# Kernel optimization log

Hardware: AMD Instinct MI355X
Metric: run time of the kernel (lower is better)

## Reference

```python
import jax, jax.numpy as jnp
import numpy as np
from jax import lax

B, S, D, NH, K = 4, 2048, 1024, 16, 3
EPS = 1e-6


def custom_layernorm(x, gamma, beta):
    # torch-style: std with ddof=1, eps added to std (not var)
    mean = jnp.mean(x, axis=-1, keepdims=True)
    var = jnp.sum((x - mean) ** 2, axis=-1, keepdims=True) / (x.shape[-1] - 1)
    std = jnp.sqrt(var)
    return gamma * ((x - mean) / (std + EPS)) + beta


def setup_inputs() -> dict:
    key = jax.random.key(0)
    ks = jax.random.split(key, 10)
    s = 1.0 / np.sqrt(D)
    return {
        "x": jax.random.normal(ks[0], (B, S, D), jnp.float32),
        "Wq": jax.random.normal(ks[1], (D, D), jnp.float32) * s,
        "bq": jax.random.normal(ks[2], (D,), jnp.float32) * 0.02,
        "Wk": jax.random.normal(ks[3], (D, D), jnp.float32) * s,
        "Wv": jax.random.normal(ks[4], (D, D), jnp.float32) * s,
        "bv": jax.random.normal(ks[5], (D,), jnp.float32) * 0.02,
        "conv_w": jax.random.normal(ks[6], (D, D // NH, K), jnp.float32) * (1.0 / np.sqrt((D // NH) * K)),
        "conv_b": jax.random.normal(ks[7], (D,), jnp.float32) * 0.02,
        "gamma": jnp.ones((D,), jnp.float32),
        "beta": jnp.zeros((D,), jnp.float32),
        "Wo": jax.random.normal(ks[8], (D, D), jnp.float32) * s,
        "bo": jax.random.normal(ks[9], (D,), jnp.float32) * 0.02,
    }


def reference(x, Wq, bq, Wk, Wv, bv, conv_w, conv_b, gamma, beta, Wo, bo):
    d = x.shape[-1]
    groups = d // conv_w.shape[1]
    pad = conv_w.shape[2] // 2

    q = x @ Wq + bq
    k = x @ Wk  # key has no bias
    v = x @ Wv + bv

    # grouped conv1d over sequence dim (NCW layout)
    xc = jnp.transpose(x, (0, 2, 1))  # [B, D, S]
    conv_out = lax.conv_general_dilated(
        xc, conv_w, window_strides=(1,), padding=[(pad, pad)],
        feature_group_count=groups,
        dimension_numbers=("NCH", "OIH", "NCH"),
    ) + conv_b[None, :, None]
    conv_out = jnp.transpose(conv_out, (0, 2, 1))  # [B, S, D]
    conv_out = custom_layernorm(conv_out, gamma, beta)  # dropout = identity (eval)

    scale = 1.0 / jnp.sqrt(jnp.asarray(d, x.dtype))
    scores = jnp.einsum("bqd,bkd->bqk", q, k) * scale  # [B, S, S]
    attn = jax.nn.softmax(scores, axis=-1)
    attention_out = jnp.einsum("bqk,bkd->bqd", attn, v)

    combined = custom_layernorm(conv_out + attention_out, gamma, beta)
    return combined @ Wo + bo + x
```

## Files before the change

kernel.cpp:

```cpp
#include <hip/hip_runtime.h>
#include <cstdint>


#define DEV __device__ __forceinline__

typedef unsigned short u16;
typedef __attribute__((ext_vector_type(8))) short bf16x8;
typedef __attribute__((ext_vector_type(4))) float f32x4;

static const int Sn = 2048, Dn = 1024;

DEV float bf2f(u16 u) { union { unsigned int i; float f; } w; w.i = ((unsigned int)u) << 16; return w.f; }
DEV u16 f2bf(float f) {
  union { float f; unsigned int i; } w; w.f = f;
  unsigned int x = w.i;
  return (u16)((x + 0x7FFFu + ((x >> 16) & 1u)) >> 16);
}

DEV void gload_lds16(const u16* gsrc, u16* lds_dst) {
  __builtin_amdgcn_global_load_lds(
      (const __attribute__((address_space(1))) void*)gsrc,
      (__attribute__((address_space(3))) void*)lds_dst,
      16, 0, 0);
}

DEV float block_allreduce_sum(float v, float* red, int tid) {
  #pragma unroll
  for (int o = 32; o > 0; o >>= 1) v += __shfl_down(v, o, 64);
  __syncthreads();
  if ((tid & 63) == 0) red[tid >> 6] = v;
  __syncthreads();
  return red[0] + red[1] + red[2] + red[3];
}

DEV float block_allreduce_max(float v, float* red, int tid) {
  #pragma unroll
  for (int o = 32; o > 0; o >>= 1) v = fmaxf(v, __shfl_down(v, o, 64));
  __syncthreads();
  if ((tid & 63) == 0) red[tid >> 6] = v;
  __syncthreads();
  return fmaxf(fmaxf(red[0], red[1]), fmaxf(red[2], red[3]));
}

__global__ __launch_bounds__(256)
void prep_all(const float* __restrict__ Wq, const float* __restrict__ Wk,
              const float* __restrict__ Wv, const float* __restrict__ Wo,
              u16* __restrict__ wT,
              const float* __restrict__ bq, const float* __restrict__ bv,
              float* __restrict__ qkvb,
              const float* __restrict__ cw, u16* __restrict__ wconv,
              const float* __restrict__ x, u16* __restrict__ xb) {
  __shared__ u16 sm[64][68];
  int blk = blockIdx.x;
  int tid = threadIdx.x;
  if (blk < 1024) {
    int w = blk >> 8, t = blk & 255;
    const float* src = (w == 0) ? Wq : (w == 1) ? Wk : (w == 2) ? Wv : Wo;
    u16* dst = wT + (size_t)w * 1048576u;
    int i0 = (t >> 4) << 6, j0 = (t & 15) << 6;
    int tx = tid & 15, r0 = tid >> 4;
    #pragma unroll
    for (int rr = r0; rr < 64; rr += 16) {
      float4 v = *(const float4*)&src[(long)(i0 + rr) * 1024 + j0 + tx * 4];
      sm[rr][tx*4+0] = f2bf(v.x); sm[rr][tx*4+1] = f2bf(v.y);
      sm[rr][tx*4+2] = f2bf(v.z); sm[rr][tx*4+3] = f2bf(v.w);
    }
    __syncthreads();
    #pragma unroll
    for (int cc = r0; cc < 64; cc += 16) {
      ushort4 o;
      o.x = sm[tx*4+0][cc]; o.y = sm[tx*4+1][cc];
      o.z = sm[tx*4+2][cc]; o.w = sm[tx*4+3][cc];
      *(ushort4*)&dst[(long)(j0 + cc) * 1024 + i0 + tx * 4] = o;
    }
  } else if (blk < 1040) {
    int oc0 = (blk - 1024) * 64;
    for (int idx = tid; idx < 64 * 192; idx += 256) {
      int oc = oc0 + idx / 192; int k = idx % 192;
      int t = k >> 6, i = k & 63;
      wconv[(long)oc * 192 + k] = f2bf(cw[(long)oc * 192 + i * 3 + t]);
    }
  } else if (blk == 1040) {
    for (int j = tid; j < 3072; j += 256) {
      float v = 0.0f;
      if (j < 1024) v = bq[j];
      else if (j >= 2048) v = bv[j - 2048];
      qkvb[j] = v;
    }
  } else {
    int i = (blk - 1041) * 1024 + tid * 4;
    float4 v = *(const float4*)&x[i];
    ushort4 o;
    o.x = f2bf(v.x); o.y = f2bf(v.y); o.z = f2bf(v.z); o.w = f2bf(v.w);
    *(ushort4*)&xb[i] = o;
  }
}

template<typename CT>
__global__ __launch_bounds__(256, 2)
void gemm_nt(const u16* __restrict__ A, const u16* __restrict__ A2, long Abs, int lda,
             const u16* __restrict__ B, long Bbs, int ldb,
             CT* __restrict__ C, CT* __restrict__ C2, long Cbs, int ldc,
             int zsplit, int K, float scale,
             const float* __restrict__ bias, int bias_bs,
             const float* __restrict__ res, long Rbs, int ldr) {
  __shared__ u16 sA[2][128 * 32];
  __shared__ u16 sB[2][128 * 32];
  int tid = threadIdx.x;
  int lane = tid & 63, wv = tid >> 6;
  int quad = lane >> 4, lm = lane & 15;
  int wr = wv >> 1, wc = wv & 1;
  long m0 = (long)blockIdx.x * 128, n0 = (long)blockIdx.y * 128;
  int z = blockIdx.z;
  if (z >= zsplit) { A = A2 + (long)(z - zsplit) * Abs; C = C2 + (long)(z - zsplit) * Cbs; }
  else             { A = A  + (long)z * Abs;            C = C  + (long)z * Cbs; }
  B += (long)z * Bbs;
  if (res) res += (long)z * Rbs;

  f32x4 acc[4][4] = {};

  int srow = wv * 16 + (lane >> 2);
  int sch = (lane & 3) * 8;
  const u16* Ap = A + (m0 + srow) * (long)lda + sch;
  const u16* Bp = B + (n0 + srow) * (long)ldb + sch;
  const int lofs = wv * 16 * 32;

  for (int k0 = 0; k0 < K; k0 += 64) {
    #pragma unroll
    for (int h = 0; h < 2; h++) {
      int kh = k0 + h * 32;
      gload_lds16(Ap + kh, &sA[h][lofs]);
      gload_lds16(Ap + 64 * (long)lda + kh, &sA[h][lofs + 64 * 32]);
      gload_lds16(Bp + kh, &sB[h][lofs]);
      gload_lds16(Bp + 64 * (long)ldb + kh, &sB[h][lofs + 64 * 32]);
    }
    __syncthreads();
    #pragma unroll
    for (int h = 0; h < 2; h++) {
      bf16x8 af[4], bfr[4];
      #pragma unroll
      for (int mi = 0; mi < 4; mi++)
        af[mi] = *(const bf16x8*)&sA[h][(wr * 64 + mi * 16 + lm) * 32 + quad * 8];
      #pragma unroll
      for (int ni = 0; ni < 4; ni++)
        bfr[ni] = *(const bf16x8*)&sB[h][(wc * 64 + ni * 16 + lm) * 32 + quad * 8];
      #pragma unroll
      for (int mi = 0; mi < 4; mi++)
        #pragma unroll
        for (int ni = 0; ni < 4; ni++)
          acc[mi][ni] = __builtin_amdgcn_mfma_f32_16x16x32_bf16(af[mi], bfr[ni], acc[mi][ni], 0, 0, 0);
    }
    __syncthreads();
  }

  #pragma unroll
  for (int mi = 0; mi < 4; mi++) {
    #pragma unroll
    for (int ni = 0; ni < 4; ni++) {
      int col = (int)n0 + wc * 64 + ni * 16 + lm;
      float bv = bias ? bias[(long)z * bias_bs + col] : 0.0f;
      #pragma unroll
      for (int r = 0; r < 4; r++) {
        long rowg = m0 + wr * 64 + mi * 16 + quad * 4 + r;
        float v = acc[mi][ni][r] * scale + bv;
        if (res) v += res[rowg * (long)ldr + col];
        if constexpr (sizeof(CT) == 2) C[rowg * (long)ldc + col] = f2bf(v);
        else                           C[rowg * (long)ldc + col] = v;
      }
    }
  }
}

__global__ __launch_bounds__(256)
void mid_all(const u16* __restrict__ xb, const u16* __restrict__ wt,
             const float* __restrict__ cb, u16* __restrict__ convo,
             const u16* __restrict__ Vb, u16* __restrict__ vt) {
  __shared__ u16 smem[9360];
  int blk = blockIdx.x;
  int tid = threadIdx.x;
  if (blk < 1024) {
    u16 (*sx)[72] = (u16(*)[72])smem;
    int s0 = (blk & 15) * 128;
    int g = (blk >> 4) & 15;
    int b = blk >> 8;
    int lane = tid & 63, wv = tid >> 6;
    int quad = lane >> 4, lm = lane & 15;
    for (int idx = tid; idx < 130 * 16; idx += 256) {
      int r = idx >> 4, c4 = (idx & 15) * 4;
      int s = s0 - 1 + r;
      ushort4 v;
      if (s >= 0 && s < Sn) v = *(const ushort4*)&xb[((long)b * Sn + s) * Dn + g * 64 + c4];
      else { v.x = 0; v.y = 0; v.z = 0; v.w = 0; }
      *(ushort4*)&sx[r][c4] = v;
    }
    __syncthreads();
    f32x4 acc[2][4] = {};
    const u16* wg = wt + (long)g * 64 * 192;
    #pragma unroll
    for (int ks = 0; ks < 6; ks++) {
      int t = ks >> 1;
      int i0 = (ks & 1) * 32 + quad * 8;
      bf16x8 a0 = *(const bf16x8*)&sx[wv * 32 + lm + t][i0];
      bf16x8 a1 = *(const bf16x8*)&sx[wv * 32 + 16 + lm + t][i0];
      #pragma unroll
      for (int nf = 0; nf < 4; nf++) {
        bf16x8 bf = *(const bf16x8*)&wg[(nf * 16 + lm) * 192 + ks * 32 + quad * 8];
        acc[0][nf] = __builtin_amdgcn_mfma_f32_16x16x32_bf16(a0, bf, acc[0][nf], 0, 0, 0);
        acc[1][nf] = __builtin_amdgcn_mfma_f32_16x16x32_bf16(a1, bf, acc[1][nf], 0, 0, 0);
      }
    }
    #pragma unroll
    for (int mi = 0; mi < 2; mi++) {
      #pragma unroll
      for (int nf = 0; nf < 4; nf++) {
        int col = g * 64 + nf * 16 + lm;
        float bias = cb[col];
        #pragma unroll
        for (int r = 0; r < 4; r++) {
          int row = wv * 32 + mi * 16 + quad * 4 + r;
          convo[((long)b * Sn + s0 + row) * Dn + col] = f2bf(acc[mi][nf][r] + bias);
        }
      }
    }
  } else {
    u16 (*sm)[68] = (u16(*)[68])smem;
    int t = blk - 1024;
    int b = t >> 9, r = t & 511;
    int j0 = (r & 15) << 6, i0 = ((r >> 4) & 31) << 6;
    const u16* s = Vb + (long)b * Sn * Dn;
    u16* d = vt + (long)b * Dn * Sn;
    int tx = tid & 15, r0 = tid >> 4;
    #pragma unroll
    for (int rr = r0; rr < 64; rr += 16) {
      ushort4 v = *(const ushort4*)&s[(long)(i0 + rr) * 1024 + j0 + tx * 4];
      sm[rr][tx*4+0] = v.x; sm[rr][tx*4+1] = v.y; sm[rr][tx*4+2] = v.z; sm[rr][tx*4+3] = v.w;
    }
    __syncthreads();
    #pragma unroll
    for (int cc = r0; cc < 64; cc += 16) {
      ushort4 o;
      o.x = sm[tx*4+0][cc]; o.y = sm[tx*4+1][cc];
      o.z = sm[tx*4+2][cc]; o.w = sm[tx*4+3][cc];
      *(ushort4*)&d[(long)(j0 + cc) * 2048 + i0 + tx * 4] = o;
    }
  }
}

__global__ __launch_bounds__(256)
void ln_kernel(const u16* __restrict__ a, const u16* __restrict__ b2,
               const float* __restrict__ gamma, const float* __restrict__ beta,
               u16* __restrict__ out) {
  __shared__ float red[4];
  long row = blockIdx.x;
  int tid = threadIdx.x;
  long base = row * Dn + tid * 4;
  ushort4 av = *(const ushort4*)&a[base];
  float v0 = bf2f(av.x), v1 = bf2f(av.y), v2 = bf2f(av.z), v3 = bf2f(av.w);
  if (b2) {
    ushort4 bv4 = *(const ushort4*)&b2[base];
    v0 += bf2f(bv4.x); v1 += bf2f(bv4.y); v2 += bf2f(bv4.z); v3 += bf2f(bv4.w);
  }
  float s = block_allreduce_sum(v0 + v1 + v2 + v3, red, tid);
  float mean = s * (1.0f / 1024.0f);
  float d0 = v0 - mean, d1 = v1 - mean, d2 = v2 - mean, d3 = v3 - mean;
  float sq = block_allreduce_sum(d0 * d0 + d1 * d1 + d2 * d2 + d3 * d3, red, tid);
  float inv = 1.0f / (sqrtf(sq * (1.0f / 1023.0f)) + 1e-6f);
  float4 gv = *(const float4*)&gamma[tid * 4];
  float4 bev = *(const float4*)&beta[tid * 4];
  ushort4 o;
  o.x = f2bf(gv.x * d0 * inv + bev.x);
  o.y = f2bf(gv.y * d1 * inv + bev.y);
  o.z = f2bf(gv.z * d2 * inv + bev.z);
  o.w = f2bf(gv.w * d3 * inv + bev.w);
  *(ushort4*)&out[base] = o;
}

__global__ __launch_bounds__(256)
void softmax_bf16(u16* __restrict__ pa, u16* __restrict__ pb, int rowsplit) {
  __shared__ float red[4];
  long row = blockIdx.x;
  u16* p = (row < rowsplit) ? pa + row * 2048 : pb + (row - rowsplit) * 2048;
  int tid = threadIdx.x;
  ushort4 a = *(const ushort4*)&p[tid * 8];
  ushort4 b = *(const ushort4*)&p[tid * 8 + 4];
  float f0 = bf2f(a.x), f1 = bf2f(a.y), f2 = bf2f(a.z), f3 = bf2f(a.w);
  float f4 = bf2f(b.x), f5 = bf2f(b.y), f6 = bf2f(b.z), f7 = bf2f(b.w);
  float m = fmaxf(fmaxf(fmaxf(f0, f1), fmaxf(f2, f3)),
                  fmaxf(fmaxf(f4, f5), fmaxf(f6, f7)));
  m = block_allreduce_max(m, red, tid);
  float e0 = __expf(f0 - m), e1 = __expf(f1 - m), e2 = __expf(f2 - m), e3 = __expf(f3 - m);
  float e4 = __expf(f4 - m), e5 = __expf(f5 - m), e6 = __expf(f6 - m), e7 = __expf(f7 - m);
  float s = block_allreduce_sum(e0 + e1 + e2 + e3 + e4 + e5 + e6 + e7, red, tid);
  float inv = 1.0f / s;
  ushort4 o1, o2;
  o1.x = f2bf(e0 * inv); o1.y = f2bf(e1 * inv); o1.z = f2bf(e2 * inv); o1.w = f2bf(e3 * inv);
  o2.x = f2bf(e4 * inv); o2.y = f2bf(e5 * inv); o2.z = f2bf(e6 * inv); o2.w = f2bf(e7 * inv);
  *(ushort4*)&p[tid * 8] = o1;
  *(ushort4*)&p[tid * 8 + 4] = o2;
}

static const size_t OFF_WT    = 0;
static const size_t OFF_QKVB  = 8ull << 20;
static const size_t OFF_WCONV = (8ull << 20) + (64 << 10);
static const size_t OFF_Q     = 9ull << 20;
static const size_t OFF_K     = 25ull << 20;
static const size_t OFF_V     = 41ull << 20;
static const size_t OFF_PW    = 57ull << 20;

extern "C" void kernel_launch(void* const* d_in, const int* in_sizes, int n_in,
                              void* d_out, int out_size, void* d_ws, size_t ws_size,
                              hipStream_t stream) {
  const float* x     = (const float*)d_in[0];
  const float* Wq    = (const float*)d_in[1];
  const float* bq    = (const float*)d_in[2];
  const float* Wk    = (const float*)d_in[3];
  const float* Wv    = (const float*)d_in[4];
  const float* bv    = (const float*)d_in[5];
  const float* cw    = (const float*)d_in[6];
  const float* cb    = (const float*)d_in[7];
  const float* gamma = (const float*)d_in[8];
  const float* beta  = (const float*)d_in[9];
  const float* Wo    = (const float*)d_in[10];
  const float* bo    = (const float*)d_in[11];
  float* out = (float*)d_out;
  char* ws = (char*)d_ws;

  u16*   wT    = (u16*)(ws + OFF_WT);
  float* qkvb  = (float*)(ws + OFF_QKVB);
  u16*   wconv = (u16*)(ws + OFF_WCONV);
  u16*   Qb    = (u16*)(ws + OFF_Q);
  u16*   Kb    = (u16*)(ws + OFF_K);
  u16*   Vb    = (u16*)(ws + OFF_V);
  u16*   Pw    = (u16*)(ws + OFF_PW);
  u16*   xb    = (u16*)d_out;
  u16*   Pd    = (u16*)d_out;
  u16*   vt    = (u16*)d_out + 8388608;
  u16*   conv  = Vb;
  u16*   attn  = Qb;
  u16*   combined = Kb;
  const long PBS = (long)Sn * Sn;

  dim3 tb(256);

  prep_all<<<dim3(9233), tb, 0, stream>>>(Wq, Wk, Wv, Wo, wT, bq, bv, qkvb,
                                          cw, wconv, x, xb);
  gemm_nt<u16><<<dim3(64, 8, 3), tb, 0, stream>>>(
      xb, nullptr, 0, 1024, wT, 1048576, 1024, Qb, (u16*)nullptr, 8388608, 1024,
      99, 1024, 1.0f, qkvb, 1024, nullptr, 0, 0);
  mid_all<<<dim3(3072), tb, 0, stream>>>(xb, wconv, cb, conv, Vb, vt);
  ln_kernel<<<dim3(8192), tb, 0, stream>>>(conv, nullptr, gamma, beta, conv);

  if (ws_size >= (73ull << 20)) {
    gemm_nt<u16><<<dim3(16, 16, 4), tb, 0, stream>>>(
        Qb, Qb + 2 * (long)Sn * Dn, (long)Sn * Dn, 1024,
        Kb, (long)Sn * Dn, 1024,
        Pd, Pw, PBS, 2048,
        2, 1024, 0.03125f, nullptr, 0, nullptr, 0, 0);
    softmax_bf16<<<dim3(8192), tb, 0, stream>>>(Pd, Pw, 4096);
    gemm_nt<u16><<<dim3(16, 8, 4), tb, 0, stream>>>(
        Pd, Pw, PBS, 2048,
        vt, (long)Dn * Sn, 2048,
        attn, attn + 2 * (long)Sn * Dn, (long)Sn * Dn, 1024,
        2, 2048, 1.0f, nullptr, 0, nullptr, 0, 0);
  } else {
    for (int c = 0; c < 2; c++) {
      long off = (long)c * 2 * Sn * Dn;
      gemm_nt<u16><<<dim3(16, 16, 2), tb, 0, stream>>>(
          Qb + off, nullptr, (long)Sn * Dn, 1024, Kb + off, (long)Sn * Dn, 1024,
          Pd, (u16*)nullptr, PBS, 2048,
          99, 1024, 0.03125f, nullptr, 0, nullptr, 0, 0);
      softmax_bf16<<<dim3(4096), tb, 0, stream>>>(Pd, Pd, 4096);
      gemm_nt<u16><<<dim3(16, 8, 2), tb, 0, stream>>>(
          Pd, nullptr, PBS, 2048, vt + off, (long)Dn * Sn, 2048,
          attn + off, (u16*)nullptr, (long)Sn * Dn, 1024,
          99, 2048, 1.0f, nullptr, 0, nullptr, 0, 0);
    }
  }

  ln_kernel<<<dim3(8192), tb, 0, stream>>>(conv, attn, gamma, beta, combined);
  gemm_nt<float><<<dim3(64, 8, 1), tb, 0, stream>>>(
      combined, nullptr, 0, 1024, wT + 3u * 1048576u, 0, 1024,
      out, (float*)nullptr, 0, 1024,
      99, 1024, 1.0f, bo, 0, x, 0, 1024);
}
```

Measured before the change: 359.4 us.

## Fuse whole pipeline into one cooperative persistent kernel with grid syncs

Replaces the chain of separate launches with a single cooperative persistent kernel of 768 blocks. Each phase (weight prep, QKV GEMM, QK^T plus V transpose, softmax plus conv, PV plus conv layernorm, final layernorm, output GEMM) is processed as a task loop and separated by grid.sync. The conv now reads fp32 x and converts weights into LDS itself, and independent work is co-scheduled within phases to remove launch gaps and tail effects. Risks include grid-sync cost, the occupancy limit from launch_bounds(256,3) with large LDS, and a fallback multi-kernel path that is used if the cooperative launch fails.

```diff
diff --git a/kernel.cpp b/kernel.cpp
--- a/kernel.cpp
+++ b/kernel.cpp
@@ -1,6 +1,9 @@
 #include <hip/hip_runtime.h>
+#include <hip/hip_cooperative_groups.h>
 #include <cstdint>
 
+
+namespace cg = cooperative_groups;
 
 #define DEV __device__ __forceinline__
 
@@ -9,6 +12,7 @@
 typedef __attribute__((ext_vector_type(4))) float f32x4;
 
 static const int Sn = 2048, Dn = 1024;
+static const long PBS = (long)Sn * Sn;
 
 DEV float bf2f(u16 u) { union { unsigned int i; float f; } w; w.i = ((unsigned int)u) << 16; return w.f; }
 DEV u16 f2bf(float f) {
@@ -42,217 +46,9 @@
   return fmaxf(fmaxf(red[0], red[1]), fmaxf(red[2], red[3]));
 }
 
-__global__ __launch_bounds__(256)
-void prep_all(const float* __restrict__ Wq, const float* __restrict__ Wk,
-              const float* __restrict__ Wv, const float* __restrict__ Wo,
-              u16* __restrict__ wT,
-              const float* __restrict__ bq, const float* __restrict__ bv,
-              float* __restrict__ qkvb,
-              const float* __restrict__ cw, u16* __restrict__ wconv,
-              const float* __restrict__ x, u16* __restrict__ xb) {
-  __shared__ u16 sm[64][68];
-  int blk = blockIdx.x;
-  int tid = threadIdx.x;
-  if (blk < 1024) {
-    int w = blk >> 8, t = blk & 255;
-    const float* src = (w == 0) ? Wq : (w == 1) ? Wk : (w == 2) ? Wv : Wo;
-    u16* dst = wT + (size_t)w * 1048576u;
-    int i0 = (t >> 4) << 6, j0 = (t & 15) << 6;
-    int tx = tid & 15, r0 = tid >> 4;
-    #pragma unroll
-    for (int rr = r0; rr < 64; rr += 16) {
-      float4 v = *(const float4*)&src[(long)(i0 + rr) * 1024 + j0 + tx * 4];
-      sm[rr][tx*4+0] = f2bf(v.x); sm[rr][tx*4+1] = f2bf(v.y);
-      sm[rr][tx*4+2] = f2bf(v.z); sm[rr][tx*4+3] = f2bf(v.w);
-    }
-    __syncthreads();
-    #pragma unroll
-    for (int cc = r0; cc < 64; cc += 16) {
-      ushort4 o;
-      o.x = sm[tx*4+0][cc]; o.y = sm[tx*4+1][cc];
-      o.z = sm[tx*4+2][cc]; o.w = sm[tx*4+3][cc];
-      *(ushort4*)&dst[(long)(j0 + cc) * 1024 + i0 + tx * 4] = o;
-    }
-  } else if (blk < 1040) {
-    int oc0 = (blk - 1024) * 64;
-    for (int idx = tid; idx < 64 * 192; idx += 256) {
-      int oc = oc0 + idx / 192; int k = idx % 192;
-      int t = k >> 6, i = k & 63;
-      wconv[(long)oc * 192 + k] = f2bf(cw[(long)oc * 192 + i * 3 + t]);
-    }
-  } else if (blk == 1040) {
-    for (int j = tid; j < 3072; j += 256) {
-      float v = 0.0f;
-      if (j < 1024) v = bq[j];
-      else if (j >= 2048) v = bv[j - 2048];
-      qkvb[j] = v;
-    }
-  } else {
-    int i = (blk - 1041) * 1024 + tid * 4;
-    float4 v = *(const float4*)&x[i];
-    ushort4 o;
-    o.x = f2bf(v.x); o.y = f2bf(v.y); o.z = f2bf(v.z); o.w = f2bf(v.w);
-    *(ushort4*)&xb[i] = o;
-  }
-}
-
-template<typename CT>
-__global__ __launch_bounds__(256, 2)
-void gemm_nt(const u16* __restrict__ A, const u16* __restrict__ A2, long Abs, int lda,
-             const u16* __restrict__ B, long Bbs, int ldb,
-             CT* __restrict__ C, CT* __restrict__ C2, long Cbs, int ldc,
-             int zsplit, int K, float scale,
-             const float* __restrict__ bias, int bias_bs,
-             const float* __restrict__ res, long Rbs, int ldr) {
-  __shared__ u16 sA[2][128 * 32];
-  __shared__ u16 sB[2][128 * 32];
-  int tid = threadIdx.x;
-  int lane = tid & 63, wv = tid >> 6;
-  int quad = lane >> 4, lm = lane & 15;
-  int wr = wv >> 1, wc = wv & 1;
-  long m0 = (long)blockIdx.x * 128, n0 = (long)blockIdx.y * 128;
-  int z = blockIdx.z;
-  if (z >= zsplit) { A = A2 + (long)(z - zsplit) * Abs; C = C2 + (long)(z - zsplit) * Cbs; }
-  else             { A = A  + (long)z * Abs;            C = C  + (long)z * Cbs; }
-  B += (long)z * Bbs;
-  if (res) res += (long)z * Rbs;
-
-  f32x4 acc[4][4] = {};
-
-  int srow = wv * 16 + (lane >> 2);
-  int sch = (lane & 3) * 8;
-  const u16* Ap = A + (m0 + srow) * (long)lda + sch;
-  const u16* Bp = B + (n0 + srow) * (long)ldb + sch;
-  const int lofs = wv * 16 * 32;
-
-  for (int k0 = 0; k0 < K; k0 += 64) {
-    #pragma unroll
-    for (int h = 0; h < 2; h++) {
-      int kh = k0 + h * 32;
-      gload_lds16(Ap + kh, &sA[h][lofs]);
-      gload_lds16(Ap + 64 * (long)lda + kh, &sA[h][lofs + 64 * 32]);
-      gload_lds16(Bp + kh, &sB[h][lofs]);
-      gload_lds16(Bp + 64 * (long)ldb + kh, &sB[h][lofs + 64 * 32]);
-    }
-    __syncthreads();
-    #pragma unroll
-    for (int h = 0; h < 2; h++) {
-      bf16x8 af[4], bfr[4];
-      #pragma unroll
-      for (int mi = 0; mi < 4; mi++)
-        af[mi] = *(const bf16x8*)&sA[h][(wr * 64 + mi * 16 + lm) * 32 + quad * 8];
-      #pragma unroll
-      for (int ni = 0; ni < 4; ni++)
-        bfr[ni] = *(const bf16x8*)&sB[h][(wc * 64 + ni * 16 + lm) * 32 + quad * 8];
-      #pragma unroll
-      for (int mi = 0; mi < 4; mi++)
-        #pragma unroll
-        for (int ni = 0; ni < 4; ni++)
-          acc[mi][ni] = __builtin_amdgcn_mfma_f32_16x16x32_bf16(af[mi], bfr[ni], acc[mi][ni], 0, 0, 0);
-    }
-    __syncthreads();
-  }
-
-  #pragma unroll
-  for (int mi = 0; mi < 4; mi++) {
-    #pragma unroll
-    for (int ni = 0; ni < 4; ni++) {
-      int col = (int)n0 + wc * 64 + ni * 16 + lm;
-      float bv = bias ? bias[(long)z * bias_bs + col] : 0.0f;
-      #pragma unroll
-      for (int r = 0; r < 4; r++) {
-        long rowg = m0 + wr * 64 + mi * 16 + quad * 4 + r;
-        float v = acc[mi][ni][r] * scale + bv;
-        if (res) v += res[rowg * (long)ldr + col];
-        if constexpr (sizeof(CT) == 2) C[rowg * (long)ldc + col] = f2bf(v);
-        else                           C[rowg * (long)ldc + col] = v;
-      }
-    }
-  }
-}
-
-__global__ __launch_bounds__(256)
-void mid_all(const u16* __restrict__ xb, const u16* __restrict__ wt,
-             const float* __restrict__ cb, u16* __restrict__ convo,
-             const u16* __restrict__ Vb, u16* __restrict__ vt) {
-  __shared__ u16 smem[9360];
-  int blk = blockIdx.x;
-  int tid = threadIdx.x;
-  if (blk < 1024) {
-    u16 (*sx)[72] = (u16(*)[72])smem;
-    int s0 = (blk & 15) * 128;
-    int g = (blk >> 4) & 15;
-    int b = blk >> 8;
-    int lane = tid & 63, wv = tid >> 6;
-    int quad = lane >> 4, lm = lane & 15;
-    for (int idx = tid; idx < 130 * 16; idx += 256) {
-      int r = idx >> 4, c4 = (idx & 15) * 4;
-      int s = s0 - 1 + r;
-      ushort4 v;
-      if (s >= 0 && s < Sn) v = *(const ushort4*)&xb[((long)b * Sn + s) * Dn + g * 64 + c4];
-      else { v.x = 0; v.y = 0; v.z = 0; v.w = 0; }
-      *(ushort4*)&sx[r][c4] = v;
-    }
-    __syncthreads();
-    f32x4 acc[2][4] = {};
-    const u16* wg = wt + (long)g * 64 * 192;
-    #pragma unroll
-    for (int ks = 0; ks < 6; ks++) {
-      int t = ks >> 1;
-      int i0 = (ks & 1) * 32 + quad * 8;
-      bf16x8 a0 = *(const bf16x8*)&sx[wv * 32 + lm + t][i0];
-      bf16x8 a1 = *(const bf16x8*)&sx[wv * 32 + 16 + lm + t][i0];
-      #pragma unroll
-      for (int nf = 0; nf < 4; nf++) {
-        bf16x8 bf = *(const bf16x8*)&wg[(nf * 16 + lm) * 192 + ks * 32 + quad * 8];
-        acc[0][nf] = __builtin_amdgcn_mfma_f32_16x16x32_bf16(a0, bf, acc[0][nf], 0, 0, 0);
-        acc[1][nf] = __builtin_amdgcn_mfma_f32_16x16x32_bf16(a1, bf, acc[1][nf], 0, 0, 0);
-      }
-    }
-    #pragma unroll
-    for (int mi = 0; mi < 2; mi++) {
-      #pragma unroll
-      for (int nf = 0; nf < 4; nf++) {
-        int col = g * 64 + nf * 16 + lm;
-        float bias = cb[col];
-        #pragma unroll
-        for (int r = 0; r < 4; r++) {
-          int row = wv * 32 + mi * 16 + quad * 4 + r;
-          convo[((long)b * Sn + s0 + row) * Dn + col] = f2bf(acc[mi][nf][r] + bias);
-        }
-      }
-    }
-  } else {
-    u16 (*sm)[68] = (u16(*)[68])smem;
-    int t = blk - 1024;
-    int b = t >> 9, r = t & 511;
-    int j0 = (r & 15) << 6, i0 = ((r >> 4) & 31) << 6;
-    const u16* s = Vb + (long)b * Sn * Dn;
-    u16* d = vt + (long)b * Dn * Sn;
-    int tx = tid & 15, r0 = tid >> 4;
-    #pragma unroll
-    for (int rr = r0; rr < 64; rr += 16) {
-      ushort4 v = *(const ushort4*)&s[(long)(i0 + rr) * 1024 + j0 + tx * 4];
-      sm[rr][tx*4+0] = v.x; sm[rr][tx*4+1] = v.y; sm[rr][tx*4+2] = v.z; sm[rr][tx*4+3] = v.w;
-    }
-    __syncthreads();
-    #pragma unroll
-    for (int cc = r0; cc < 64; cc += 16) {
-      ushort4 o;
-      o.x = sm[tx*4+0][cc]; o.y = sm[tx*4+1][cc];
-      o.z = sm[tx*4+2][cc]; o.w = sm[tx*4+3][cc];
-      *(ushort4*)&d[(long)(j0 + cc) * 2048 + i0 + tx * 4] = o;
-    }
-  }
-}
-
-__global__ __launch_bounds__(256)
-void ln_kernel(const u16* __restrict__ a, const u16* __restrict__ b2,
-               const float* __restrict__ gamma, const float* __restrict__ beta,
-               u16* __restrict__ out) {
-  __shared__ float red[4];
-  long row = blockIdx.x;
-  int tid = threadIdx.x;
+DEV void ln_row(const u16* __restrict__ a, const u16* __restrict__ b2,
+                const float* __restrict__ gamma, const float* __restrict__ beta,
+                u16* __restrict__ out, long row, int tid, float* red) {
   long base = row * Dn + tid * 4;
   ushort4 av = *(const ushort4*)&a[base];
   float v0 = bf2f(av.x), v1 = bf2f(av.y), v2 = bf2f(av.z), v3 = bf2f(av.w);
@@ -275,12 +71,7 @@
   *(ushort4*)&out[base] = o;
 }
 
-__global__ __launch_bounds__(256)
-void softmax_bf16(u16* __restrict__ pa, u16* __restrict__ pb, int rowsplit) {
-  __shared__ float red[4];
-  long row = blockIdx.x;
-  u16* p = (row < rowsplit) ? pa + row * 2048 : pb + (row - rowsplit) * 2048;
-  int tid = threadIdx.x;
+DEV void softmax_row(u16* __restrict__ p, int tid, float* red) {
   ushort4 a = *(const ushort4*)&p[tid * 8];
   ushort4 b = *(const ushort4*)&p[tid * 8 + 4];
   float f0 = bf2f(a.x), f1 = bf2f(a.y), f2 = bf2f(a.z), f3 = bf2f(a.w);
@@ -299,13 +90,368 @@
   *(ushort4*)&p[tid * 8 + 4] = o2;
 }
 
-static const size_t OFF_WT    = 0;
-static const size_t OFF_QKVB  = 8ull << 20;
-static const size_t OFF_WCONV = (8ull << 20) + (64 << 10);
-static const size_t OFF_Q     = 9ull << 20;
-static const size_t OFF_K     = 25ull << 20;
-static const size_t OFF_V     = 41ull << 20;
-static const size_t OFF_PW    = 57ull << 20;
+template<typename CT>
+DEV void gemm_tile(u16* sm, int tid,
+                   const u16* __restrict__ A, int lda,
+                   const u16* __restrict__ B, int ldb,
+                   CT* __restrict__ C, int ldc,
+                   long m0, long n0, int K, float scale,
+                   const float* __restrict__ bias,
+                   const float* __restrict__ res, int ldr) {
+  u16* sA = sm;
+  u16* sB = sm + 8192;
+  int lane = tid & 63, wv = tid >> 6;
+  int quad = lane >> 4, lm = lane & 15;
+  int wr = wv >> 1, wc = wv & 1;
+  f32x4 acc[4][4] = {};
+  int srow = wv * 16 + (lane >> 2);
+  int sch = (lane & 3) * 8;
+  const u16* Ap = A + (m0 + srow) * (long)lda + sch;
+  const u16* Bp = B + (n0 + srow) * (long)ldb + sch;
+  const int lofs = wv * 16 * 32;
+
+  for (int k0 = 0; k0 < K; k0 += 64) {
+    #pragma unroll
+    for (int h = 0; h < 2; h++) {
+      int kh = k0 + h * 32;
+      gload_lds16(Ap + kh, &sA[h * 4096 + lofs]);
+      gload_lds16(Ap + 64 * (long)lda + kh, &sA[h * 4096 + lofs + 64 * 32]);
+      gload_lds16(Bp + kh, &sB[h * 4096 + lofs]);
+      gload_lds16(Bp + 64 * (long)ldb + kh, &sB[h * 4096 + lofs + 64 * 32]);
+    }
+    __syncthreads();
+    #pragma unroll
+    for (int h = 0; h < 2; h++) {
+      bf16x8 af[4], bfr[4];
+      #pragma unroll
+      for (int mi = 0; mi < 4; mi++)
+        af[mi] = *(const bf16x8*)&sA[h * 4096 + (wr * 64 + mi * 16 + lm) * 32 + quad * 8];
+      #pragma unroll
+      for (int ni = 0; ni < 4; ni++)
+        bfr[ni] = *(const bf16x8*)&sB[h * 4096 + (wc * 64 + ni * 16 + lm) * 32 + quad * 8];
+      #pragma unroll
+      for (int mi = 0; mi < 4; mi++)
+        #pragma unroll
+        for (int ni = 0; ni < 4; ni++)
+          acc[mi][ni] = __builtin_amdgcn_mfma_f32_16x16x32_bf16(af[mi], bfr[ni], acc[mi][ni], 0, 0, 0);
+    }
+    __syncthreads();
+  }
+  #pragma unroll
+  for (int mi = 0; mi < 4; mi++) {
+    #pragma unroll
+    for (int ni = 0; ni < 4; ni++) {
+      int col = (int)n0 + wc * 64 + ni * 16 + lm;
+      float bv = bias ? bias[col] : 0.0f;
+      #pragma unroll
+      for (int r = 0; r < 4; r++) {
+        long rowg = m0 + wr * 64 + mi * 16 + quad * 4 + r;
+        float v = acc[mi][ni][r] * scale + bv;
+        if (res) v += res[rowg * (long)ldr + col];
+        if constexpr (sizeof(CT) == 2) C[rowg * (long)ldc + col] = f2bf(v);
+        else                           C[rowg * (long)ldc + col] = v;
+      }
+    }
+  }
+}
+
+DEV void wtr_task(u16* sm_, int tid, int t4,
+                  const float* __restrict__ Wq, const float* __restrict__ Wk,
+                  const float* __restrict__ Wv, const float* __restrict__ Wo,
+                  u16* __restrict__ wT) {
+  u16 (*sm)[68] = (u16(*)[68])sm_;
+  int w = t4 >> 8, t = t4 & 255;
+  const float* src = (w == 0) ? Wq : (w == 1) ? Wk : (w == 2) ? Wv : Wo;
+  u16* dst = wT + (size_t)w * 1048576u;
+  int i0 = (t >> 4) << 6, j0 = (t & 15) << 6;
+  int tx = tid & 15, r0 = tid >> 4;
+  #pragma unroll
+  for (int rr = r0; rr < 64; rr += 16) {
+    float4 v = *(const float4*)&src[(long)(i0 + rr) * 1024 + j0 + tx * 4];
+    sm[rr][tx*4+0] = f2bf(v.x); sm[rr][tx*4+1] = f2bf(v.y);
+    sm[rr][tx*4+2] = f2bf(v.z); sm[rr][tx*4+3] = f2bf(v.w);
+  }
+  __syncthreads();
+  #pragma unroll
+  for (int cc = r0; cc < 64; cc += 16) {
+    ushort4 o;
+    o.x = sm[tx*4+0][cc]; o.y = sm[tx*4+1][cc];
+    o.z = sm[tx*4+2][cc]; o.w = sm[tx*4+3][cc];
+    *(ushort4*)&dst[(long)(j0 + cc) * 1024 + i0 + tx * 4] = o;
+  }
+  __syncthreads();
+}
+
+DEV void vt_task(u16* sm_, int tid, int tt,
+                 const u16* __restrict__ Vb, u16* __restrict__ vt) {
+  u16 (*sm)[68] = (u16(*)[68])sm_;
+  int b = tt >> 9, r = tt & 511;
+  int j0 = (r & 15) << 6, i0 = ((r >> 4) & 31) << 6;
+  const u16* s = Vb + (long)b * Sn * Dn;
+  u16* d = vt + (long)b * Dn * Sn;
+  int tx = tid & 15, r0 = tid >> 4;
+  #pragma unroll
+  for (int rr = r0; rr < 64; rr += 16) {
+    ushort4 v = *(const ushort4*)&s[(long)(i0 + rr) * 1024 + j0 + tx * 4];
+    sm[rr][tx*4+0] = v.x; sm[rr][tx*4+1] = v.y; sm[rr][tx*4+2] = v.z; sm[rr][tx*4+3] = v.w;
+  }
+  __syncthreads();
+  #pragma unroll
+  for (int cc = r0; cc < 64; cc += 16) {
+    ushort4 o;
+    o.x = sm[tx*4+0][cc]; o.y = sm[tx*4+1][cc];
+    o.z = sm[tx*4+2][cc]; o.w = sm[tx*4+3][cc];
+    *(ushort4*)&d[(long)(j0 + cc) * 2048 + i0 + tx * 4] = o;
+  }
+  __syncthreads();
+}
+
+DEV void conv_task(u16* smem, int tid, int r,
+                   const float* __restrict__ x, const float* __restrict__ cw,
+                   const float* __restrict__ cb, u16* __restrict__ convo) {
+  u16 (*sx)[72] = (u16(*)[72])smem;
+  u16 (*sw)[200] = (u16(*)[200])(smem + 9360);
+  int s0 = (r & 15) * 128;
+  int g = (r >> 4) & 15;
+  int b = r >> 8;
+  int lane = tid & 63, wv = tid >> 6;
+  int quad = lane >> 4, lm = lane & 15;
+  for (int idx = tid; idx < 64 * 192; idx += 256) {
+    int oc = idx / 192, k = idx - oc * 192;
+    int t = k >> 6, i = k & 63;
+    sw[oc][k] = f2bf(cw[((long)(g * 64 + oc)) * 192 + i * 3 + t]);
+  }
+  for (int idx = tid; idx < 130 * 16; idx += 256) {
+    int rr = idx >> 4, c4 = (idx & 15) * 4;
+    int s = s0 - 1 + rr;
+    ushort4 v;
+    if (s >= 0 && s < Sn) {
+      float4 f = *(const float4*)&x[((long)b * Sn + s) * Dn + g * 64 + c4];
+      v.x = f2bf(f.x); v.y = f2bf(f.y); v.z = f2bf(f.z); v.w = f2bf(f.w);
+    } else { v.x = 0; v.y = 0; v.z = 0; v.w = 0; }
+    *(ushort4*)&sx[rr][c4] = v;
+  }
+  __syncthreads();
+  f32x4 acc[2][4] = {};
+  #pragma unroll
+  for (int ks = 0; ks < 6; ks++) {
+    int t = ks >> 1;
+    int i0 = (ks & 1) * 32 + quad * 8;
+    bf16x8 a0 = *(const bf16x8*)&sx[wv * 32 + lm + t][i0];
+    bf16x8 a1 = *(const bf16x8*)&sx[wv * 32 + 16 + lm + t][i0];
+    #pragma unroll
+    for (int nf = 0; nf < 4; nf++) {
+      bf16x8 bf = *(const bf16x8*)&sw[nf * 16 + lm][ks * 32 + quad * 8];
+      acc[0][nf] = __builtin_amdgcn_mfma_f32_16x16x32_bf16(a0, bf, acc[0][nf], 0, 0, 0);
+      acc[1][nf] = __builtin_amdgcn_mfma_f32_16x16x32_bf16(a1, bf, acc[1][nf], 0, 0, 0);
+    }
+  }
+  #pragma unroll
+  for (int mi = 0; mi < 2; mi++) {
+    #pragma unroll
+    for (int nf = 0; nf < 4; nf++) {
+      int col = g * 64 + nf * 16 + lm;
+      float bias = cb[col];
+      #pragma unroll
+      for (int rr = 0; rr < 4; rr++) {
+        int row = wv * 32 + mi * 16 + quad * 4 + rr;
+        convo[((long)b * Sn + s0 + row) * Dn + col] = f2bf(acc[mi][nf][rr] + bias);
+      }
+    }
+  }
+  __syncthreads();
+}
+
+struct MegaP {
+  const float *x, *Wq, *bq, *Wk, *Wv, *bv, *cw, *cb, *gamma, *beta, *Wo, *bo;
+  u16 *wT; float *qkvb;
+  u16 *Qb, *Kb, *Vb, *Pw, *xb, *Pd, *vt, *conv, *attn, *combined;
+  float *out;
+};
+
+__global__ __launch_bounds__(256, 3)
+void mega(MegaP P) {
+  __shared__ u16 smem[22168];
+  __shared__ float red[4];
+  cg::grid_group grid = cg::this_grid();
+  int tid = threadIdx.x;
+  int nb = gridDim.x;
+
+  for (int t = blockIdx.x; t < 9217; t += nb) {
+    if (t < 1024) {
+      wtr_task(smem, tid, t, P.Wq, P.Wk, P.Wv, P.Wo, P.wT);
+    } else if (t == 1024) {
+      for (int j = tid; j < 3072; j += 256) {
+        float v = 0.0f;
+        if (j < 1024) v = P.bq[j];
+        else if (j >= 2048) v = P.bv[j - 2048];
+        P.qkvb[j] = v;
+      }
+    } else {
+      int i = (t - 1025) * 1024 + tid * 4;
+      float4 v = *(const float4*)&P.x[i];
+      ushort4 o;
+      o.x = f2bf(v.x); o.y = f2bf(v.y); o.z = f2bf(v.z); o.w = f2bf(v.w);
+      *(ushort4*)&P.xb[i] = o;
+    }
+  }
+  grid.sync();
+  for (int t = blockIdx.x; t < 1536; t += nb) {
+    int z = t >> 9, r = t & 511;
+    gemm_tile<u16>(smem, tid, P.xb, 1024, P.wT + (size_t)z * 1048576u, 1024,
+                   P.Qb + (long)z * 8388608, 1024,
+                   (long)(r & 63) * 128, (long)(r >> 6) * 128, 1024, 1.0f,
+                   P.qkvb + z * 1024, nullptr, 0);
+  }
+  grid.sync();
+  for (int t = blockIdx.x; t < 3072; t += nb) {
+    if (t < 1024) {
+      int z = t >> 8, r = t & 255;
+      u16* C = (z < 2) ? P.Pd + (long)z * PBS : P.Pw + (long)(z - 2) * PBS;
+      gemm_tile<u16>(smem, tid, P.Qb + (long)z * Sn * Dn, 1024,
+                     P.Kb + (long)z * Sn * Dn, 1024, C, 2048,
+                     (long)(r & 15) * 128, (long)((r >> 4) & 15) * 128,
+                     1024, 0.03125f, nullptr, nullptr, 0);
+    } else {
+      vt_task(smem, tid, t - 1024, P.Vb, P.vt);
+    }
+  }
+  grid.sync();
+  for (int t = blockIdx.x; t < 9216; t += nb) {
+    if (t < 8192) {
+      u16* p = (t < 4096) ? P.Pd + (long)t * 2048 : P.Pw + (long)(t - 4096) * 2048;
+      softmax_row(p, tid, red);
+    } else {
+      conv_task(smem, tid, t - 8192, P.x, P.cw, P.cb, P.conv);
+    }
+  }
+  grid.sync();
+  for (int t = blockIdx.x; t < 8704; t += nb) {
+    if (t < 512) {
+      int z = t >> 7, r = t & 127;
+      const u16* A = (z < 2) ? P.Pd + (long)z * PBS : P.Pw + (long)(z - 2) * PBS;
+      gemm_tile<u16>(smem, tid, A, 2048, P.vt + (long)z * Dn * Sn, 2048,
+                     P.attn + (long)z * Sn * Dn, 1024,
+                     (long)(r & 15) * 128, (long)((r >> 4) & 7) * 128,
+                     2048, 1.0f, nullptr, nullptr, 0);
+    } else {
+      ln_row(P.conv, nullptr, P.gamma, P.beta, P.conv, t - 512, tid, red);
+    }
+  }
+  grid.sync();
+  for (int t = blockIdx.x; t < 8192; t += nb)
+    ln_row(P.conv, P.attn, P.gamma, P.beta, P.combined, t, tid, red);
+  grid.sync();
+  for (int t = blockIdx.x; t < 512; t += nb)
+    gemm_tile<float>(smem, tid, P.combined, 1024, P.wT + 3u * 1048576u, 1024,
+                     P.out, 1024, (long)(t & 63) * 128, (long)(t >> 6) * 128,
+                     1024, 1.0f, P.bo, P.x, 1024);
+}
+
+__global__ __launch_bounds__(256)
+void prep_all(const float* Wq, const float* Wk, const float* Wv, const float* Wo,
+              u16* wT, const float* bq, const float* bv, float* qkvb,
+              const float* x, u16* xb) {
+  __shared__ u16 sm[4352];
+  int blk = blockIdx.x, tid = threadIdx.x;
+  if (blk < 1024) {
+    wtr_task(sm, tid, blk, Wq, Wk, Wv, Wo, wT);
+  } else if (blk == 1024) {
+    for (int j = tid; j < 3072; j += 256) {
+      float v = 0.0f;
+      if (j < 1024) v = bq[j];
+      else if (j >= 2048) v = bv[j - 2048];
+      qkvb[j] = v;
+    }
+  } else {
+    int i = (blk - 1025) * 1024 + tid * 4;
+    float4 v = *(const float4*)&x[i];
+    ushort4 o;
+    o.x = f2bf(v.x); o.y = f2bf(v.y); o.z = f2bf(v.z); o.w = f2bf(v.w);
+    *(ushort4*)&xb[i] = o;
+  }
+}
+
+template<typename CT>
+__global__ __launch_bounds__(256, 2)
+void gemm_nt(const u16* A, const u16* A2, long Abs, int lda,
+             const u16* B, long Bbs, int ldb,
+             CT* C, CT* C2, long Cbs, int ldc,
+             int zsplit, int K, float scale,
+             const float* bias, int bias_bs,
+             const float* res, long Rbs, int ldr) {
+  __shared__ u16 sm[16384];
+  int z = blockIdx.z;
+  if (z >= zsplit) { A = A2 + (long)(z - zsplit) * Abs; C = C2 + (long)(z - zsplit) * Cbs; }
+  else             { A = A  + (long)z * Abs;            C = C  + (long)z * Cbs; }
+  gemm_tile<CT>(sm, threadIdx.x, A, lda, B + (long)z * Bbs, ldb, C, ldc,
+                (long)blockIdx.x * 128, (long)blockIdx.y * 128, K, scale,
+                bias ? bias + (long)z * bias_bs : nullptr,
+                res ? res + (long)z * Rbs : nullptr, ldr);
+}
+
+__global__ __launch_bounds__(256, 2)
+void post_qkv(int ngemm, const u16* Qb, const u16* Kb,
+              u16* Pd, u16* Pw, const u16* Vb, u16* vt) {
+  __shared__ u16 sm[16384];
+  int blk = blockIdx.x, tid = threadIdx.x;
+  if (blk < ngemm) {
+    int z = blk >> 8, r = blk & 255;
+    u16* C = (z < 2) ? Pd + (long)z * PBS : Pw + (long)(z - 2) * PBS;
+    gemm_tile<u16>(sm, tid, Qb + (long)z * Sn * Dn, 1024,
+                   Kb + (long)z * Sn * Dn, 1024, C, 2048,
+                   (long)(r & 15) * 128, (long)((r >> 4) & 15) * 128,
+                   1024, 0.03125f, nullptr, nullptr, 0);
+  } else {
+    vt_task(sm, tid, blk - ngemm, Vb, vt);
+  }
+}
+
+__global__ __launch_bounds__(256)
+void smax_conv(u16* pa, u16* pb, int rowsplit, int nsm,
+               const float* x, const float* cw, const float* cb, u16* convo) {
+  __shared__ u16 smem[22168];
+  __shared__ float red[4];
+  int blk = blockIdx.x, tid = threadIdx.x;
+  if (blk < nsm) {
+    u16* p = (blk < rowsplit) ? pa + (long)blk * 2048 : pb + (long)(blk - rowsplit) * 2048;
+    softmax_row(p, tid, red);
+  } else {
+    conv_task(smem, tid, blk - nsm, x, cw, cb, convo);
+  }
+}
+
+__global__ __launch_bounds__(256, 2)
+void pv_ln(int npv, const u16* Pd, const u16* Pw, const u16* vt, u16* attn,
+           u16* conv, const float* gamma, const float* beta) {
+  __shared__ u16 sm[16384];
+  __shared__ float red[4];
+  int blk = blockIdx.x, tid = threadIdx.x;
+  if (blk < npv) {
+    int z = blk >> 7, r = blk & 127;
+    const u16* A = (z < 2) ? Pd + (long)z * PBS : Pw + (long)(z - 2) * PBS;
+    gemm_tile<u16>(sm, tid, A, 2048, vt + (long)z * Dn * Sn, 2048,
+                   attn + (long)z * Sn * Dn, 1024,
+                   (long)(r & 15) * 128, (long)((r >> 4) & 7) * 128,
+                   2048, 1.0f, nullptr, nullptr, 0);
+  } else {
+    ln_row(conv, nullptr, gamma, beta, conv, blk - npv, tid, red);
+  }
+}
+
+__global__ __launch_bounds__(256)
+void ln_kernel(const u16* a, const u16* b2, const float* gamma,
+               const float* beta, u16* out) {
+  __shared__ float red[4];
+  ln_row(a, b2, gamma, beta, out, blockIdx.x, threadIdx.x, red);
+}
+
+static const size_t OFF_WT   = 0;
+static const size_t OFF_QKVB = 8ull << 20;
+static const size_t OFF_Q    = 9ull << 20;
+static const size_t OFF_K    = 25ull << 20;
+static const size_t OFF_V    = 41ull << 20;
+static const size_t OFF_PW   = 57ull << 20;
 
 extern "C" void kernel_launch(void* const* d_in, const int* in_sizes, int n_in,
                               void* d_out, int out_size, void* d_ws, size_t ws_size,
@@ -327,7 +473,6 @@
 
   u16*   wT    = (u16*)(ws + OFF_WT);
   float* qkvb  = (float*)(ws + OFF_QKVB);
-  u16*   wconv = (u16*)(ws + OFF_WCONV);
   u16*   Qb    = (u16*)(ws + OFF_Q);
   u16*   Kb    = (u16*)(ws + OFF_K);
   u16*   Vb    = (u16*)(ws + OFF_V);
@@ -338,48 +483,44 @@
   u16*   conv  = Vb;
   u16*   attn  = Qb;
   u16*   combined = Kb;
-  const long PBS = (long)Sn * Sn;
 
   dim3 tb(256);
 
-  prep_all<<<dim3(9233), tb, 0, stream>>>(Wq, Wk, Wv, Wo, wT, bq, bv, qkvb,
-                                          cw, wconv, x, xb);
+  hipError_t cerr = hipErrorUnknown;
+  if (ws_size >= (73ull << 20)) {
+    MegaP P{x, Wq, bq, Wk, Wv, bv, cw, cb, gamma, beta, Wo, bo,
+            wT, qkvb, Qb, Kb, Vb, Pw, xb, Pd, vt, conv, attn, combined, out};
+    void* args[] = { &P };
+    cerr = hipLaunchCooperativeKernel((const void*)mega, dim3(768), tb, args, 0, stream);
+  }
+  if (cerr == hipSuccess) return;
+
+  prep_all<<<dim3(9217), tb, 0, stream>>>(Wq, Wk, Wv, Wo, wT, bq, bv, qkvb, x, xb);
   gemm_nt<u16><<<dim3(64, 8, 3), tb, 0, stream>>>(
       xb, nullptr, 0, 1024, wT, 1048576, 1024, Qb, (u16*)nullptr, 8388608, 1024,
       99, 1024, 1.0f, qkvb, 1024, nullptr, 0, 0);
-  mid_all<<<dim3(3072), tb, 0, stream>>>(xb, wconv, cb, conv, Vb, vt);
-  ln_kernel<<<dim3(8192), tb, 0, stream>>>(conv, nullptr, gamma, beta, conv);
-
   if (ws_size >= (73ull << 20)) {
-    gemm_nt<u16><<<dim3(16, 16, 4), tb, 0, stream>>>(
-        Qb, Qb + 2 * (long)Sn * Dn, (long)Sn * Dn, 1024,
-        Kb, (long)Sn * Dn, 1024,
-        Pd, Pw, PBS, 2048,
-        2, 1024, 0.03125f, nullptr, 0, nullptr, 0, 0);
-    softmax_bf16<<<dim3(8192), tb, 0, stream>>>(Pd, Pw, 4096);
-    gemm_nt<u16><<<dim3(16, 8, 4), tb, 0, stream>>>(
-        Pd, Pw, PBS, 2048,
-        vt, (long)Dn * Sn, 2048,
-        attn, attn + 2 * (long)Sn * Dn, (long)Sn * Dn, 1024,
-        2, 2048, 1.0f, nullptr, 0, nullptr, 0, 0);
+    post_qkv<<<dim3(1024 + 2048), tb, 0, stream>>>(1024, Qb, Kb, Pd, Pw, Vb, vt);
+    smax_conv<<<dim3(8192 + 1024), tb, 0, stream>>>(Pd, Pw, 4096, 8192, x, cw, cb, conv);
+    pv_ln<<<dim3(512 + 8192), tb, 0, stream>>>(512, Pd, Pw, vt, attn, conv, gamma, beta);
   } else {
+    post_qkv<<<dim3(2048), tb, 0, stream>>>(0, Qb, Kb, Pd, Pw, Vb, vt);
     for (int c = 0; c < 2; c++) {
       long off = (long)c * 2 * Sn * Dn;
       gemm_nt<u16><<<dim3(16, 16, 2), tb, 0, stream>>>(
           Qb + off, nullptr, (long)Sn * Dn, 1024, Kb + off, (long)Sn * Dn, 1024,
-          Pd, (u16*)nullptr, PBS, 2048,
-          99, 1024, 0.03125f, nullptr, 0, nullptr, 0, 0);
-      softmax_bf16<<<dim3(4096), tb, 0, stream>>>(Pd, Pd, 4096);
+          Pd, (u16*)nullptr, PBS, 2048, 99, 1024, 0.03125f, nullptr, 0, nullptr, 0, 0);
+      smax_conv<<<dim3(4096 + (c == 0 ? 1024 : 0)), tb, 0, stream>>>(
+          Pd, Pd, 4096, 4096, x, cw, cb, conv);
       gemm_nt<u16><<<dim3(16, 8, 2), tb, 0, stream>>>(
           Pd, nullptr, PBS, 2048, vt + off, (long)Dn * Sn, 2048,
           attn + off, (u16*)nullptr, (long)Sn * Dn, 1024,
           99, 2048, 1.0f, nullptr, 0, nullptr, 0, 0);
     }
-  }
-
+    ln_kernel<<<dim3(8192), tb, 0, stream>>>(conv, nullptr, gamma, beta, conv);
+  }
   ln_kernel<<<dim3(8192), tb, 0, stream>>>(conv, attn, gamma, beta, combined);
   gemm_nt<float><<<dim3(64, 8, 1), tb, 0, stream>>>(
       combined, nullptr, 0, 1024, wT + 3u * 1048576u, 0, 1024,
-      out, (float*)nullptr, 0, 1024,
-      99, 1024, 1.0f, bo, 0, x, 0, 1024);
-}
+      out, (float*)nullptr, 0, 1024, 99, 1024, 1.0f, bo, 0, x, 0, 1024);
+}
```

After: 938.2 us. +161.1%, slower.
